# Kernel optimization log

Hardware: AMD Instinct MI355X
Metric: run time of the kernel (lower is better)

## Reference

```python
import jax, jax.numpy as jnp
import numpy as np

K = 8          # opt.pk, explicit precision cutoff
MARGIN = 0.2   # opt.margin
NEG = -1e30    # sentinel for masked sort keys


def setup_inputs() -> dict:
    key = jax.random.key(0)
    k1, k2 = jax.random.split(key)
    batch_reprs = jax.random.normal(k1, (4096, 512), dtype=jnp.float32)
    batch_labels = jax.random.randint(k2, (4096,), 0, 64)
    return {"batch_reprs": batch_reprs, "batch_labels": batch_labels}


def _forward(batch_reprs, batch_labels):
    B = batch_reprs.shape[0]
    dt = batch_reprs.dtype
    # cls_match_mat: 1 if same class
    match = (batch_labels[:, None] == batch_labels[None, :]).astype(dt)
    # pairwise euclidean distance (squared=False), safe sqrt at zero diagonal
    sq = jnp.sum(batch_reprs * batch_reprs, axis=1)
    res = jnp.maximum(sq[:, None] - 2.0 * (batch_reprs @ batch_reprs.T) + sq[None, :], 0.0)
    zero = res <= 0.0
    d = jnp.where(zero, 0.0, jnp.sqrt(jnp.where(zero, 1.0, res)))
    sim_hat = -d + (1.0 - match) * MARGIN  # use_margin=True path
    # rank via double argsort (descending similarity -> rank 1 = best)
    order = jnp.argsort(-sim_hat, axis=1)
    rank = jnp.argsort(order, axis=1).astype(dt) + 1.0
    pos_nums = jnp.sum(match, axis=1)
    ks = jnp.minimum(pos_nums, jnp.asarray(K + 1, dt))[:, None]  # k_mat per row
    w = 1.0 / jnp.log2(rank + 1.0) + 1.0  # DCG-style rank weight
    # false positives: not same class, within top-k_i
    fp_mask = (match < 1.0) & (rank <= ks)
    fp_nums = jnp.sum(fp_mask, axis=1)  # |N| per row
    # false negatives: same class, beyond top-k_i
    fn_mask = (match > 0.0) & (rank > ks)
    fp_term = jnp.sum(jnp.where(fp_mask, sim_hat * w, 0.0))
    # per-row variable-size topk over false negatives, vectorized:
    # mask non-FN entries to -inf, sort desc, keep first fp_nums[i] entries
    fn_key = jnp.where(fn_mask, sim_hat, NEG)
    fn_order = jnp.argsort(-fn_key, axis=1)
    sorted_sim = jnp.take_along_axis(sim_hat, fn_order, axis=1)
    sorted_w = jnp.take_along_axis(w, fn_order, axis=1)
    sorted_valid = jnp.take_along_axis(fn_mask, fn_order, axis=1)
    take = (jnp.arange(B)[None, :].astype(dt) < fp_nums[:, None]) & sorted_valid
    fn_term = jnp.sum(jnp.where(take, sorted_sim * sorted_w, 0.0))
    # rows with fp_num==0 contribute 0 to both terms, matching the host loop
    return fp_term - fn_term


def reference(batch_reprs, batch_labels):
    return _forward(batch_reprs, batch_labels)
```

## Files before the change

### kernel.cpp

```cpp
#include <hip/hip_runtime.h>
#include <math.h>

#define BB 4096
#define DD 512
#define KTOP 9
#define MARGIN_F 0.2f
#define NT 32
#define NTRI (NT * (NT + 1) / 2)

typedef __attribute__((ext_vector_type(8))) short short8;
typedef __attribute__((ext_vector_type(4))) float f32x4;
typedef unsigned long long u64;

__device__ unsigned short g_Rhi[(size_t)BB * DD];
__device__ unsigned short g_Rpk[(size_t)BB * DD];
__device__ u64 g_cmask[64 * 64];

__device__ __forceinline__ unsigned short f2bf(float x) {
  unsigned u = __float_as_uint(x);
  u += 0x7fffu + ((u >> 16) & 1u);
  return (unsigned short)(u >> 16);
}

__device__ __forceinline__ float ord16val(unsigned o16) {
  unsigned e = (o16 << 16) | 0x8000u;
  unsigned s = (e & 0x80000000u) ? (e ^ 0x80000000u) : ~e;
  return __uint_as_float(s);
}

__device__ __forceinline__ unsigned wavemax32_dpp(unsigned c) {
#define MSTEP(CTRL, RM)                                                        \
  {                                                                            \
    unsigned o = (unsigned)__builtin_amdgcn_update_dpp(0, (int)c, CTRL, RM, 0xf, false); \
    if (o > c) c = o;                                                          \
  }
  MSTEP(0xB1, 0xf) MSTEP(0x4E, 0xf) MSTEP(0x141, 0xf) MSTEP(0x140, 0xf)
  MSTEP(0x142, 0xa) MSTEP(0x143, 0xc)
#undef MSTEP
  return (unsigned)__builtin_amdgcn_readlane((int)c, 63);
}

__device__ __forceinline__ int wavesum_dpp(int c) {
#define SSTEP(CTRL, RM)                                                        \
  c += __builtin_amdgcn_update_dpp(0, c, CTRL, RM, 0xf, false);
  SSTEP(0xB1, 0xf) SSTEP(0x4E, 0xf) SSTEP(0x141, 0xf) SSTEP(0x140, 0xf)
  SSTEP(0x142, 0xa) SSTEP(0x143, 0xc)
#undef SSTEP
  return __builtin_amdgcn_readlane(c, 63);
}

__device__ __forceinline__ unsigned u4c(const uint4& f, int q) {
  return q == 0 ? f.x : q == 1 ? f.y : q == 2 ? f.z : f.w;
}

__global__ __launch_bounds__(64) void splitsq(const float* __restrict__ R,
                                              float* __restrict__ sq) {
  const int row = blockIdx.x, lane = threadIdx.x;
  const float4* r4 = (const float4*)(R + (size_t)row * DD);
  float4 a = r4[lane], b = r4[lane + 64];
  float xs[8] = {a.x, a.y, a.z, a.w, b.x, b.y, b.z, b.w};
  unsigned short hs[8];
  float s = 0.f;
  #pragma unroll
  for (int q = 0; q < 8; ++q) {
    float x = xs[q];
    s += x * x;
    hs[q] = f2bf(x);
  }
  const size_t base = (size_t)row * DD;
  *(ushort4*)&g_Rhi[base + lane * 4]       = *(ushort4*)&hs[0];
  *(ushort4*)&g_Rhi[base + 256 + lane * 4] = *(ushort4*)&hs[4];
  #pragma unroll
  for (int off = 32; off; off >>= 1) s += __shfl_down(s, off);
  if (lane == 0) sq[row] = s;
}

__global__ __launch_bounds__(256) void repack(void) {
  const int p = blockIdx.x;
  #pragma unroll
  for (int i = 0; i < 4; ++i) {
    const int idx = i * 256 + threadIdx.x;
    const int ks = idx >> 6, l = idx & 63;
    const int row = p * 16 + (l & 15);
    const int k0 = ks * 32 + (l >> 4) * 8;
    *(uint4*)&g_Rpk[(size_t)p * 8192 + (size_t)idx * 8] =
        *(const uint4*)&g_Rhi[(size_t)row * DD + k0];
  }
}

__global__ __launch_bounds__(64) void buildmask(const int* __restrict__ labels) {
  __shared__ int slab[BB];
  const int c = blockIdx.x, lane = threadIdx.x;
  for (int i = lane; i < BB / 4; i += 64) ((int4*)slab)[i] = ((const int4*)labels)[i];
  __syncthreads();
  u64 m = 0;
  #pragma unroll
  for (int e = 0; e < 64; ++e) {
    int j = 512 * (e >> 3) + 8 * lane + (e & 7);
    m |= (u64)(slab[j] == c) << e;
  }
  g_cmask[c * 64 + lane] = m;
}

__global__ __launch_bounds__(256, 2) void simgemm_pk(const int* __restrict__ labels,
                                                     const float* __restrict__ sq,
                                                     unsigned short* __restrict__ simq) {
  const int x = blockIdx.x & 7;
  int c = blockIdx.x >> 3;
  int bi = 0, bj = 0;
  #pragma unroll
  for (int q = 0; q < 4; ++q) {
    const int bjq = (q < 2) ? (2 * x + q) : (28 - 2 * x + q);
    const int n = bjq + 1;
    if (c >= 0 && c < n) { bj = bjq; bi = c; }
    c -= n;
  }
  const int i0 = bi * 128, j0 = bj * 128;

  __shared__ __align__(16) unsigned char smembytes[35840];

  const int tid = threadIdx.x;
  const int wid = tid >> 6, lane = tid & 63;
  const int wr = wid >> 1, wc = wid & 1;
  const int lrow = lane & 15, kblk = lane >> 4;

  const unsigned short* pA[4];
  const unsigned short* pB[4];
  #pragma unroll
  for (int m = 0; m < 4; ++m) {
    pA[m] = g_Rpk + (size_t)(bi * 8 + wr * 4 + m) * 8192 + lane * 8;
    pB[m] = g_Rpk + (size_t)(bj * 8 + wc * 4 + m) * 8192 + lane * 8;
  }

  f32x4 acc[4][4] = {};
  short8 fa[2][4], fb[2][4];

  #pragma unroll
  for (int m = 0; m < 4; ++m) {
    fa[0][m] = *(const short8*)(pA[m]);
    fb[0][m] = *(const short8*)(pB[m]);
  }

  #pragma unroll
  for (int step = 0; step < 16; ++step) {
    const int cur = step & 1;
    if (step < 15) {
      const int koff = (step + 1) * 512;
      #pragma unroll
      for (int m = 0; m < 4; ++m) {
        fa[cur ^ 1][m] = *(const short8*)(pA[m] + koff);
        fb[cur ^ 1][m] = *(const short8*)(pB[m] + koff);
      }
    }
    #pragma unroll
    for (int m = 0; m < 4; ++m) {
      #pragma unroll
      for (int n = 0; n < 4; ++n) {
        acc[m][n] = __builtin_amdgcn_mfma_f32_16x16x32_bf16(fa[cur][m], fb[cur][n], acc[m][n], 0, 0, 0);
      }
    }
  }

  unsigned short (*T)[132] = (unsigned short (*)[132])smembytes;
  float* sqi = (float*)(smembytes + 33792);
  float* sqj = (float*)(smembytes + 34304);
  int* labi  = (int*)(smembytes + 34816);
  int* labj  = (int*)(smembytes + 35328);
  if (tid < 128) { sqi[tid] = sq[i0 + tid]; labi[tid] = labels[i0 + tid]; }
  else { int t2 = tid - 128; sqj[t2] = sq[j0 + t2]; labj[t2] = labels[j0 + t2]; }
  __syncthreads();

  #pragma unroll
  for (int m = 0; m < 4; ++m) {
    const int rbase = wr * 64 + m * 16 + kblk * 4;
    #pragma unroll
    for (int n = 0; n < 4; ++n) {
      const int ccol = wc * 64 + n * 16 + lrow;
      const float sqc = sqj[ccol];
      const int lc_ = labj[ccol];
      #pragma unroll
      for (int reg = 0; reg < 4; ++reg) {
        const int r = rbase + reg;
        float res = sqi[r] - 2.0f * acc[m][n][reg] + sqc;
        float dd = (res <= 0.f) ? 0.f : sqrtf(res);
        float sv = -dd + ((labi[r] != lc_) ? MARGIN_F : 0.f);
        unsigned su = __float_as_uint(sv);
        unsigned ord = su ^ ((unsigned)((int)su >> 31) | 0x80000000u);
        T[r][ccol] = (unsigned short)(ord >> 16);
      }
    }
  }
  __syncthreads();

  const int srow0 = tid >> 4, scol0 = (tid & 15) * 8;
  #pragma unroll
  for (int p = 0; p < 8; ++p) {
    const int r = p * 16 + srow0;
    short8 w = *(const short8*)&T[r][scol0];
    *(short8*)&simq[(size_t)(i0 + r) * BB + j0 + scol0] = w;
  }
  if (bi != bj) {
    #pragma unroll
    for (int p = 0; p < 8; ++p) {
      const int col = p * 16 + srow0;
      unsigned short tmp[8];
      #pragma unroll
      for (int t = 0; t < 8; ++t) tmp[t] = T[scol0 + t][col];
      *(short8*)&simq[(size_t)(j0 + col) * BB + i0 + scol0] = *(short8*)tmp;
    }
  }
}

#define TOP2UPD(k, a, b) {                                                     \
  unsigned _mx = ((k) > (a)) ? (k) : (a);                                      \
  unsigned _mn = ((k) > (a)) ? (a) : (k);                                      \
  (a) = _mx;                                                                   \
  (b) = (_mn > (b)) ? _mn : (b); }

__global__ __launch_bounds__(128) void rowproc9(const unsigned short* __restrict__ simq,
                                                const int* __restrict__ labels,
                                                float* __restrict__ partials) {
  __shared__ unsigned sred[2 * KTOP + 2][2];
  __shared__ int sint[2 + 2 * KTOP];

  const int tid = threadIdx.x;
  const int lane = tid & 63;
  const int h = tid >> 6;
  const int row = blockIdx.x;

  const uint4* rp = (const uint4*)(simq + (size_t)row * BB);
  uint4 w0 = rp[lane + (4 * h + 0) * 64];
  uint4 w1 = rp[lane + (4 * h + 1) * 64];
  uint4 w2 = rp[lane + (4 * h + 2) * 64];
  uint4 w3 = rp[lane + (4 * h + 3) * 64];

  const int myl = labels[row];
  const unsigned mh = (unsigned)(g_cmask[myl * 64 + lane] >> (32 * h));
  const unsigned lbase2 = (unsigned)((4095 - 8 * lane) << 1);

  unsigned k[32];
  #pragma unroll
  for (int s = 0; s < 4; ++s) {
    const uint4 w = s == 0 ? w0 : s == 1 ? w1 : s == 2 ? w2 : w3;
    const unsigned base_s = lbase2 - (unsigned)(1024 * (4 * h + s));
    #pragma unroll
    for (int q = 0; q < 4; ++q) {
      const unsigned wv = u4c(w, q);
      const int e0 = s * 8 + q * 2;
      k[e0]     = ((wv & 0xffffu) << 13)
                | (base_s - (unsigned)((q * 2) << 1)     + ((mh >> e0) & 1u));
      k[e0 + 1] = ((wv >> 16) << 13)
                | (base_s - (unsigned)((q * 2 + 1) << 1) + ((mh >> (e0 + 1)) & 1u));
    }
  }

  {
    int p = wavesum_dpp(__popc(mh));
    sint[h] = p;
  }
  __syncthreads();
  const int pos = sint[0] + sint[1];
  const int ks = min(pos, KTOP);

  unsigned h1 = 0, h2 = 0;
  #pragma unroll
  for (int e = 0; e < 32; ++e) TOP2UPD(k[e], h1, h2);

  unsigned kth = 0;
  float fp = 0.f; int fpn = 0;
  #pragma unroll
  for (int t = 0; t < KTOP; ++t) {
    if (t < ks) {
      sred[t][h] = wavemax32_dpp(h1);
    }
    __syncthreads();
    if (t < ks) {
      const unsigned g = max(sred[t][0], sred[t][1]);
      if (!(g & 1u)) { fp += ord16val(g >> 13) * (1.f / log2f((float)(t + 2)) + 1.f); fpn++; }
      if (t == ks - 1) kth = g;
      if (h1 == g) {
        h1 = h2; h2 = ~0u;
        if (h1 == ~0u) {
          h1 = 0; h2 = 0;
          #pragma unroll
          for (int e = 0; e < 32; ++e) {
            if (k[e] < g) TOP2UPD(k[e], h1, h2);
          }
        }
      }
    }
  }

  float fn = 0.f;
  if (fpn > 0) {
    unsigned f1 = 0, f2 = 0;
    #pragma unroll
    for (int e = 0; e < 32; ++e) {
      if ((k[e] & 1u) && k[e] < kth) TOP2UPD(k[e], f1, f2);
    }
    unsigned ck[KTOP];
    int nc = 0;
    #pragma unroll
    for (int u = 0; u < KTOP; ++u) {
      ck[u] = ~0u;
      if (u < fpn) {
        sred[KTOP + 1 + u][h] = wavemax32_dpp(f1);
      }
      __syncthreads();
      if (u < fpn) {
        const unsigned g = max(sred[KTOP + 1 + u][0], sred[KTOP + 1 + u][1]);
        if (g != 0u) {
          ck[u] = g; nc = u + 1;
          if (f1 == g) {
            f1 = f2; f2 = ~0u;
            if (f1 == ~0u) {
              f1 = 0; f2 = 0;
              #pragma unroll
              for (int e = 0; e < 32; ++e) {
                if ((k[e] & 1u) && k[e] < g) TOP2UPD(k[e], f1, f2);
              }
            }
          }
        }
      }
    }
    if (nc > 0) {
      int cnt[KTOP];
      #pragma unroll
      for (int u = 0; u < KTOP; ++u) cnt[u] = 0;
      #pragma unroll
      for (int e = 0; e < 32; ++e) {
        #pragma unroll
        for (int u = 0; u < KTOP; ++u) cnt[u] += (k[e] > ck[u]) ? 1 : 0;
      }
      #pragma unroll
      for (int u = 0; u < KTOP; ++u) {
        sint[2 + h * KTOP + u] = wavesum_dpp(cnt[u]);
      }
    }
    __syncthreads();
    if (nc > 0) {
      #pragma unroll
      for (int u = 0; u < KTOP; ++u) {
        if (u < nc) {
          const int rank = 1 + sint[2 + u] + sint[2 + KTOP + u];
          fn += ord16val(ck[u] >> 13) * (1.f / log2f((float)(rank + 1)) + 1.f);
        }
      }
    }
  }

  if (tid == 0) partials[row] = fp - fn;
}

__global__ __launch_bounds__(256) void finalreduce(const float* __restrict__ partials,
                                                   float* __restrict__ out) {
  __shared__ float s[256];
  const int tid = threadIdx.x;
  float acc = 0.f;
  for (int j = tid; j < BB; j += 256) acc += partials[j];
  s[tid] = acc; __syncthreads();
  #pragma unroll
  for (int st = 128; st; st >>= 1) { if (tid < st) s[tid] += s[tid + st]; __syncthreads(); }
  if (tid == 0) out[0] = s[0];
}

extern "C" void kernel_launch(void* const* d_in, const int* in_sizes, int n_in,
                              void* d_out, int out_size, void* d_ws, size_t ws_size,
                              hipStream_t stream) {
  const float* R      = (const float*)d_in[0];
  const int*   labels = (const int*)d_in[1];
  float* out = (float*)d_out;

  unsigned short* simq = (unsigned short*)d_ws;
  float* sq            = (float*)((char*)d_ws + (size_t)BB * BB * 2);
  float* partials      = sq + BB;

  splitsq<<<BB, 64, 0, stream>>>(R, sq);
  repack<<<BB / 16, 256, 0, stream>>>();
  buildmask<<<64, 64, 0, stream>>>(labels);
  simgemm_pk<<<NTRI, 256, 0, stream>>>(labels, sq, simq);
  rowproc9<<<BB, 128, 0, stream>>>(simq, labels, partials);
  finalreduce<<<1, 256, 0, stream>>>(partials, out);
}
```

Baseline: 89.08 us.

## Compute per-wave top-k independently and merge lists after a single barrier

The row kernel previously synchronized both waves on every top-k extraction step to combine the per-wave maxima. Now each wave extracts its own top-9 (and top-fpn false negatives) locally with DPP reductions, writes the sorted lists to shared memory, and the two lists are merged after one barrier. This removes many block-wide syncs per row, in exchange for some redundant extraction iterations beyond ks.

Result: no change. 90.76 us (+1.9%).

```diff
diff --git a/kernel.cpp b/kernel.cpp
--- a/kernel.cpp
+++ b/kernel.cpp
@@ -217,11 +217,13 @@
   (a) = _mx;                                                                   \
   (b) = (_mn > (b)) ? _mn : (b); }
 
-__global__ __launch_bounds__(128) void rowproc9(const unsigned short* __restrict__ simq,
-                                                const int* __restrict__ labels,
-                                                float* __restrict__ partials) {
-  __shared__ unsigned sred[2 * KTOP + 2][2];
-  __shared__ int sint[2 + 2 * KTOP];
+__global__ __launch_bounds__(128) void rowproc10(const unsigned short* __restrict__ simq,
+                                                 const int* __restrict__ labels,
+                                                 float* __restrict__ partials) {
+  __shared__ unsigned sl[2][KTOP];
+  __shared__ unsigned sf[2][KTOP];
+  __shared__ int spos[2];
+  __shared__ int scnt[2][KTOP];
 
   const int tid = threadIdx.x;
   const int lane = tid & 63;
@@ -256,37 +258,44 @@
 
   {
     int p = wavesum_dpp(__popc(mh));
-    sint[h] = p;
+    if (lane == 0) spos[h] = p;
+  }
+
+  unsigned h1 = 0, h2 = 0;
+  #pragma unroll
+  for (int e = 0; e < 32; ++e) TOP2UPD(k[e], h1, h2);
+  #pragma unroll
+  for (int t = 0; t < KTOP; ++t) {
+    const unsigned g = wavemax32_dpp(h1);
+    if (lane == 0) sl[h][t] = g;
+    if (h1 == g) {
+      h1 = h2; h2 = ~0u;
+      if (h1 == ~0u) {
+        h1 = 0; h2 = 0;
+        #pragma unroll
+        for (int e = 0; e < 32; ++e) {
+          if (k[e] < g) TOP2UPD(k[e], h1, h2);
+        }
+      }
+    }
   }
   __syncthreads();
-  const int pos = sint[0] + sint[1];
+
+  const int pos = spos[0] + spos[1];
   const int ks = min(pos, KTOP);
 
-  unsigned h1 = 0, h2 = 0;
-  #pragma unroll
-  for (int e = 0; e < 32; ++e) TOP2UPD(k[e], h1, h2);
-
-  unsigned kth = 0;
-  float fp = 0.f; int fpn = 0;
-  #pragma unroll
-  for (int t = 0; t < KTOP; ++t) {
-    if (t < ks) {
-      sred[t][h] = wavemax32_dpp(h1);
-    }
-    __syncthreads();
-    if (t < ks) {
-      const unsigned g = max(sred[t][0], sred[t][1]);
-      if (!(g & 1u)) { fp += ord16val(g >> 13) * (1.f / log2f((float)(t + 2)) + 1.f); fpn++; }
-      if (t == ks - 1) kth = g;
-      if (h1 == g) {
-        h1 = h2; h2 = ~0u;
-        if (h1 == ~0u) {
-          h1 = 0; h2 = 0;
-          #pragma unroll
-          for (int e = 0; e < 32; ++e) {
-            if (k[e] < g) TOP2UPD(k[e], h1, h2);
-          }
-        }
+  float fp = 0.f; int fpn = 0; unsigned kth = 0;
+  {
+    int ia = 0, ib = 0;
+    #pragma unroll
+    for (int t = 0; t < KTOP; ++t) {
+      if (t < ks) {
+        const unsigned va = (ia < KTOP) ? sl[0][ia] : 0u;
+        const unsigned vb = (ib < KTOP) ? sl[1][ib] : 0u;
+        unsigned m;
+        if (va >= vb) { m = va; ++ia; } else { m = vb; ++ib; }
+        if (!(m & 1u)) { fp += ord16val(m >> 13) * (1.f / log2f((float)(t + 2)) + 1.f); fpn++; }
+        if (t == ks - 1) kth = m;
       }
     }
   }
@@ -298,31 +307,41 @@
     for (int e = 0; e < 32; ++e) {
       if ((k[e] & 1u) && k[e] < kth) TOP2UPD(k[e], f1, f2);
     }
-    unsigned ck[KTOP];
-    int nc = 0;
     #pragma unroll
     for (int u = 0; u < KTOP; ++u) {
-      ck[u] = ~0u;
+      unsigned g = 0;
       if (u < fpn) {
-        sred[KTOP + 1 + u][h] = wavemax32_dpp(f1);
-      }
-      __syncthreads();
-      if (u < fpn) {
-        const unsigned g = max(sred[KTOP + 1 + u][0], sred[KTOP + 1 + u][1]);
-        if (g != 0u) {
-          ck[u] = g; nc = u + 1;
-          if (f1 == g) {
-            f1 = f2; f2 = ~0u;
-            if (f1 == ~0u) {
-              f1 = 0; f2 = 0;
-              #pragma unroll
-              for (int e = 0; e < 32; ++e) {
-                if ((k[e] & 1u) && k[e] < g) TOP2UPD(k[e], f1, f2);
-              }
+        g = wavemax32_dpp(f1);
+        if (g != 0u && f1 == g) {
+          f1 = f2; f2 = ~0u;
+          if (f1 == ~0u) {
+            f1 = 0; f2 = 0;
+            #pragma unroll
+            for (int e = 0; e < 32; ++e) {
+              if ((k[e] & 1u) && k[e] < g) TOP2UPD(k[e], f1, f2);
             }
           }
         }
       }
+      if (lane == 0) sf[h][u] = g;
+    }
+    __syncthreads();
+
+    unsigned ck[KTOP];
+    int nc = 0;
+    {
+      int ia = 0, ib = 0;
+      #pragma unroll
+      for (int u = 0; u < KTOP; ++u) {
+        ck[u] = ~0u;
+        if (u < fpn) {
+          const unsigned va = (ia < KTOP) ? sf[0][ia] : 0u;
+          const unsigned vb = (ib < KTOP) ? sf[1][ib] : 0u;
+          unsigned m;
+          if (va >= vb) { m = va; ++ia; } else { m = vb; ++ib; }
+          if (m != 0u) { ck[u] = m; nc = u + 1; }
+        }
+      }
     }
     if (nc > 0) {
       int cnt[KTOP];
@@ -335,7 +354,8 @@
       }
       #pragma unroll
       for (int u = 0; u < KTOP; ++u) {
-        sint[2 + h * KTOP + u] = wavesum_dpp(cnt[u]);
+        const int sc_ = wavesum_dpp(cnt[u]);
+        if (lane == 0) scnt[h][u] = sc_;
       }
     }
     __syncthreads();
@@ -343,7 +363,7 @@
       #pragma unroll
       for (int u = 0; u < KTOP; ++u) {
         if (u < nc) {
-          const int rank = 1 + sint[2 + u] + sint[2 + KTOP + u];
+          const int rank = 1 + scnt[0][u] + scnt[1][u];
           fn += ord16val(ck[u] >> 13) * (1.f / log2f((float)(rank + 1)) + 1.f);
         }
       }
@@ -380,6 +400,6 @@
   repack<<<BB / 16, 256, 0, stream>>>();
   buildmask<<<64, 64, 0, stream>>>(labels);
   simgemm_pk<<<NTRI, 256, 0, stream>>>(labels, sq, simq);
-  rowproc9<<<BB, 128, 0, stream>>>(simq, labels, partials);
+  rowproc10<<<BB, 128, 0, stream>>>(simq, labels, partials);
   finalreduce<<<1, 256, 0, stream>>>(partials, out);
 }
```
